# Kernel tuning notes

Measured on AMD Instinct MI355X. Metric: run time of the kernel, lower is better.

Reference implementation:

```python
import jax, jax.numpy as jnp
import numpy as np

N, E, B = 50000, 800000, 64
IN, H, OUT = 64, 128, 64


def _gcn_norm(edge_index, num_nodes):
    # PyG gcn_norm with add_self_loops=True: A_hat = A + I, norm = d^-1/2[src]*d^-1/2[dst]
    loop = jnp.arange(num_nodes)
    src = jnp.concatenate([edge_index[0], loop])
    dst = jnp.concatenate([edge_index[1], loop])
    deg = jax.ops.segment_sum(jnp.ones_like(dst, dtype=jnp.float32), dst,
                              num_segments=num_nodes)  # >= 1 due to self-loops
    dis = deg ** -0.5
    norm = dis[src] * dis[dst]  # [E+N]
    return src, dst, norm


def _gcn_layer(x, W, b, src, dst, norm, num_nodes):
    h = x @ W                                   # linear first (GCNConv order)
    msg = h[src] * norm[:, None]                # gather + normalize, [E+N, H]
    out = jax.ops.segment_sum(msg, dst, num_segments=num_nodes)  # scatter-add
    return out + b


def setup_inputs() -> dict:
    key = jax.random.key(0)
    ks = jax.random.split(key, 12)
    x = jax.random.normal(ks[0], (N, IN), dtype=jnp.float32)
    edge_index = jax.random.randint(ks[1], (2, E), 0, N, dtype=jnp.int64)
    batch = jnp.sort(jax.random.randint(ks[2], (N,), 0, B, dtype=jnp.int64))

    def lin(k, fan_in, fan_out):
        s = 1.0 / np.sqrt(fan_in)
        return jax.random.uniform(k, (fan_in, fan_out), jnp.float32, -s, s)

    return {
        "x": x, "edge_index": edge_index, "batch": batch,
        "W1": lin(ks[3], IN, H), "b1": jnp.zeros((H,), jnp.float32),
        "W2": lin(ks[4], H, H),  "b2": jnp.zeros((H,), jnp.float32),
        "W3": lin(ks[5], H, H),  "b3": jnp.zeros((H,), jnp.float32),
        "W4": lin(ks[6], H, OUT), "b4": jnp.zeros((OUT,), jnp.float32),
    }


def reference(x, edge_index, batch, W1, b1, W2, b2, W3, b3, W4, b4):
    src, dst, norm = _gcn_norm(edge_index, N)
    h = jax.nn.relu(_gcn_layer(x, W1, b1, src, dst, norm, N))
    h = jax.nn.relu(_gcn_layer(h, W2, b2, src, dst, norm, N))
    # global mean pool over graphs
    sums = jax.ops.segment_sum(h, batch, num_segments=B)          # [B, H]
    cnts = jax.ops.segment_sum(jnp.ones((N,), jnp.float32), batch, num_segments=B)
    pooled = sums / jnp.maximum(cnts, 1.0)[:, None]
    # MLP head
    return jax.nn.relu(pooled @ W3 + b3) @ W4 + b4                # [B, OUT]
```

## Files before the change

kernel.cpp:

```cpp
#include <hip/hip_runtime.h>


__device__ __forceinline__ float ldf(const void* p, long long i, int f32) {
    if (f32) return ((const float*)p)[i];
    unsigned int u = ((const unsigned short*)p)[i];
    return __uint_as_float(u << 16);
}
__device__ __forceinline__ float bfl(unsigned int u) { return __uint_as_float(u << 16); }
__device__ __forceinline__ float bfh(unsigned int u) { return __uint_as_float(u & 0xFFFF0000u); }
__device__ __forceinline__ int ld_idx(const int* p, long long i, int i64) {
    return i64 ? p[2 * i] : p[i];
}
__device__ __forceinline__ unsigned short f2bf(float v) {
    unsigned int x = __float_as_uint(v);
    return (unsigned short)((x + 0x7FFFu + ((x >> 16) & 1u)) >> 16);
}
__device__ __forceinline__ int clampi(int v, int lo, int hi) {
    return v < lo ? lo : (v > hi ? hi : v);
}

#define OW1 0
#define OB1 8192
#define OW2 8320
#define OB2 24704
#define OW3 24832
#define OB3 41216
#define OW4 41344
#define OB4 49536
#define OTOT 49600


__global__ void gnn_prep(const void* W1, const void* b1, const void* W2, const void* b2,
                         const void* W3, const void* b3, const void* W4, const void* b4,
                         const int* __restrict__ ei,
                         int* __restrict__ flags_out,
                         int* __restrict__ degcnt, float* __restrict__ pooled,
                         float* __restrict__ wsW, int N, int B) {
    __shared__ int s_cnt, s_or;
    const int t = threadIdx.x;
    if (t == 0) { s_cnt = 0; s_or = 0; }
    __syncthreads();
    {
        const unsigned int* w1w = (const unsigned int*)W1;
        int c = 0, o = 0;
        for (int i = t; i < 512; i += 256) {
            unsigned int e = (w1w[i] >> 7) & 0xFFu;
            if (e >= 100 && e <= 140) c++;
        }
        for (int i = t; i < 1024; i += 256) o |= ei[2 * i + 1];
        atomicAdd(&s_cnt, c);
        atomicOr(&s_or, o);
    }
    __syncthreads();
    const int f32 = (s_cnt > 256) ? 0 : 1;
    if (blockIdx.x == 0 && t == 0) {
        flags_out[0] = f32;
        flags_out[1] = (s_or == 0) ? 1 : 0;
    }
    const int i = blockIdx.x * 256 + t;
    const int stride = gridDim.x * 256;
    for (int j = i; j < N; j += stride) degcnt[j] = 0;
    for (int j = i; j < B * 128; j += stride) pooled[j] = 0.f;
    for (int j = i; j < OTOT; j += stride) {
        float v;
        if      (j < OB1) v = ldf(W1, j - OW1, f32);
        else if (j < OW2) v = ldf(b1, j - OB1, f32);
        else if (j < OB2) v = ldf(W2, j - OW2, f32);
        else if (j < OW3) v = ldf(b2, j - OB2, f32);
        else if (j < OB3) v = ldf(W3, j - OW3, f32);
        else if (j < OW4) v = ldf(b3, j - OB3, f32);
        else if (j < OB4) v = ldf(W4, j - OW4, f32);
        else              v = ldf(b4, j - OB4, f32);
        wsW[j] = v;
    }
}


__global__ void gnn_hist(const int* __restrict__ ei, int E, int N,
                         const int* __restrict__ flags, int* __restrict__ degcnt,
                         int* __restrict__ rank) {
    int base = (blockIdx.x * 256 + threadIdx.x) * 4;
    if (base >= E) return;
    int i64 = flags[1];
    int m = min(4, E - base);
    int d[4], r[4];
#pragma unroll
    for (int j = 0; j < 4; ++j)
        if (j < m) d[j] = clampi(ld_idx(ei, (long long)E + base + j, i64), 0, N - 1);
#pragma unroll
    for (int j = 0; j < 4; ++j)
        if (j < m) r[j] = atomicAdd(&degcnt[d[j]], 1);
#pragma unroll
    for (int j = 0; j < 4; ++j)
        if (j < m) rank[base + j] = r[j];
}

__global__ void gnn_scan1(const int* __restrict__ cnt, int* __restrict__ excl,
                          int* __restrict__ sums, float* __restrict__ dis, int N) {
    __shared__ int sh[256];
    int t = threadIdx.x;
    int i = blockIdx.x * 256 + t;
    int v = (i < N) ? cnt[i] : 0;
    sh[t] = v;
    __syncthreads();
    for (int off = 1; off < 256; off <<= 1) {
        int a = (t >= off) ? sh[t - off] : 0;
        __syncthreads();
        sh[t] += a;
        __syncthreads();
    }
    if (i < N) {
        excl[i] = sh[t] - v;
        dis[i] = rsqrtf((float)v + 1.0f);
    }
    if (t == 255) sums[blockIdx.x] = sh[255];
}

__global__ void gnn_scan2(int* __restrict__ sums, int nb) {
    __shared__ int sh[256];
    int t = threadIdx.x;
    int v = (t < nb) ? sums[t] : 0;
    sh[t] = v;
    __syncthreads();
    for (int off = 1; off < 256; off <<= 1) {
        int a = (t >= off) ? sh[t - off] : 0;
        __syncthreads();
        sh[t] += a;
        __syncthreads();
    }
    if (t < nb) sums[t] = sh[t] - v;
}

template <bool SMALLN>
__global__ void gnn_fill(const int* __restrict__ ei, const int* __restrict__ excl,
                         const int* __restrict__ bsums, const int* __restrict__ rank,
                         void* __restrict__ csr, int E, int N,
                         const int* __restrict__ flags,
                         const void* __restrict__ x, const float* __restrict__ dis,
                         unsigned short* __restrict__ xb) {
    const int tid = blockIdx.x * 256 + threadIdx.x;
    const int i64 = flags[1];
    if (tid < E) {
        int s = clampi(ld_idx(ei, (long long)tid, i64), 0, N - 1);
        int d = clampi(ld_idx(ei, (long long)E + tid, i64), 0, N - 1);
        int pos = excl[d] + bsums[d >> 8] + rank[tid];
        if (SMALLN) ((unsigned short*)csr)[pos] = (unsigned short)s;
        else        ((int*)csr)[pos] = s;
    }
    const int f32 = flags[0];
    const int total = N * 16;
    const int stride = gridDim.x * 256;
    for (int j = tid; j < total; j += stride) {
        int n = j >> 4;
        float dn = dis[n];
        float v0, v1, v2, v3;
        if (f32) {
            float4 xv = ((const float4*)x)[j];
            v0 = xv.x; v1 = xv.y; v2 = xv.z; v3 = xv.w;
        } else {
            ushort4 xv = ((const ushort4*)x)[j];
            v0 = bfl(xv.x); v1 = bfl(xv.y); v2 = bfl(xv.z); v3 = bfl(xv.w);
        }
        ushort4 o;
        o.x = f2bf(v0 * dn); o.y = f2bf(v1 * dn);
        o.z = f2bf(v2 * dn); o.w = f2bf(v3 * dn);
        ((ushort4*)xb)[j] = o;
    }
}

template <bool SMALLN>
__device__ __forceinline__ int csr_at(const void* csr, int e) {
    return SMALLN ? (int)((const unsigned short*)csr)[e] : ((const int*)csr)[e];
}


template <bool SMALLN>
__global__ __launch_bounds__(128) void gnn_l1(const unsigned short* __restrict__ xb,
                                              const int* __restrict__ excl,
                                              const int* __restrict__ bsums,
                                              const void* __restrict__ csr,
                                              const float* __restrict__ dis,
                                              const float* __restrict__ W1,
                                              const float* __restrict__ b1,
                                              int N, int E,
                                              unsigned short* __restrict__ H1b) {
    __shared__ float Xs[16 * 64];
    const int t = threadIdx.x;
    const int nbase = blockIdx.x * 16;
    const int wave = t >> 6;
    const int lane = t & 63;
    const int eslot = lane >> 3;
    const int fg = lane & 7;

    for (int pass = 0; pass < 8; ++pass) {
        const int ln = pass * 2 + wave;
        const int n = nbase + ln;
        float a0 = 0.f, a1 = 0.f, a2 = 0.f, a3 = 0.f;
        float a4 = 0.f, a5 = 0.f, a6 = 0.f, a7 = 0.f;
        if (n < N) {
            int beg = excl[n] + bsums[n >> 8];
            int end = (n + 1 < N) ? (excl[n + 1] + bsums[(n + 1) >> 8]) : E;
            for (int e = beg + eslot; e < end; e += 8) {
                int s = csr_at<SMALLN>(csr, e);
                uint4 u = *(const uint4*)(xb + (long long)s * 64 + fg * 8);
                a0 += bfl(u.x); a1 += bfh(u.x);
                a2 += bfl(u.y); a3 += bfh(u.y);
                a4 += bfl(u.z); a5 += bfh(u.z);
                a6 += bfl(u.w); a7 += bfh(u.w);
            }
        }
#pragma unroll
        for (int m = 8; m <= 32; m <<= 1) {
            a0 += __shfl_xor(a0, m); a1 += __shfl_xor(a1, m);
            a2 += __shfl_xor(a2, m); a3 += __shfl_xor(a3, m);
            a4 += __shfl_xor(a4, m); a5 += __shfl_xor(a5, m);
            a6 += __shfl_xor(a6, m); a7 += __shfl_xor(a7, m);
        }
        if (n < N && eslot == 0) {
            float dn = dis[n];
            uint4 u = *(const uint4*)(xb + (long long)n * 64 + fg * 8);
            float4 o0, o1;
            o0.x = (a0 + bfl(u.x)) * dn; o0.y = (a1 + bfh(u.x)) * dn;
            o0.z = (a2 + bfl(u.y)) * dn; o0.w = (a3 + bfh(u.y)) * dn;
            o1.x = (a4 + bfl(u.z)) * dn; o1.y = (a5 + bfh(u.z)) * dn;
            o1.z = (a6 + bfl(u.w)) * dn; o1.w = (a7 + bfh(u.w)) * dn;
            *(float4*)&Xs[ln * 64 + fg * 8]     = o0;
            *(float4*)&Xs[ln * 64 + fg * 8 + 4] = o1;
        } else if (n >= N && eslot == 0) {
            float4 z = make_float4(0.f, 0.f, 0.f, 0.f);
            *(float4*)&Xs[ln * 64 + fg * 8]     = z;
            *(float4*)&Xs[ln * 64 + fg * 8 + 4] = z;
        }
    }
    __syncthreads();

    const int fgB = t & 31, ng = t >> 5;
    const int f0 = fgB * 4, n0 = ng * 4;
    const float4* Xs4 = (const float4*)Xs;
    const float4* Wp  = (const float4*)W1;
    float4 acc[4];
#pragma unroll
    for (int j = 0; j < 4; ++j) acc[j] = make_float4(0.f, 0.f, 0.f, 0.f);
#pragma unroll 4
    for (int k4 = 0; k4 < 16; ++k4) {
        const float4 wa = Wp[(4 * k4 + 0) * 32 + fgB];
        const float4 wb = Wp[(4 * k4 + 1) * 32 + fgB];
        const float4 wc = Wp[(4 * k4 + 2) * 32 + fgB];
        const float4 wd = Wp[(4 * k4 + 3) * 32 + fgB];
#pragma unroll
        for (int j = 0; j < 4; ++j) {
            const float4 xv = Xs4[(n0 + j) * 16 + k4];
            acc[j].x = fmaf(xv.x, wa.x, acc[j].x); acc[j].y = fmaf(xv.x, wa.y, acc[j].y);
            acc[j].z = fmaf(xv.x, wa.z, acc[j].z); acc[j].w = fmaf(xv.x, wa.w, acc[j].w);
            acc[j].x = fmaf(xv.y, wb.x, acc[j].x); acc[j].y = fmaf(xv.y, wb.y, acc[j].y);
            acc[j].z = fmaf(xv.y, wb.z, acc[j].z); acc[j].w = fmaf(xv.y, wb.w, acc[j].w);
            acc[j].x = fmaf(xv.z, wc.x, acc[j].x); acc[j].y = fmaf(xv.z, wc.y, acc[j].y);
            acc[j].z = fmaf(xv.z, wc.z, acc[j].z); acc[j].w = fmaf(xv.z, wc.w, acc[j].w);
            acc[j].x = fmaf(xv.w, wd.x, acc[j].x); acc[j].y = fmaf(xv.w, wd.y, acc[j].y);
            acc[j].z = fmaf(xv.w, wd.z, acc[j].z); acc[j].w = fmaf(xv.w, wd.w, acc[j].w);
        }
    }
    const float4 b = *(const float4*)&b1[f0];
#pragma unroll
    for (int j = 0; j < 4; ++j) {
        int n = nbase + n0 + j;
        if (n >= N) continue;
        const float dn = dis[n];
        float4 a = acc[j];
        a.x = fmaxf(a.x + b.x, 0.f) * dn;
        a.y = fmaxf(a.y + b.y, 0.f) * dn;
        a.z = fmaxf(a.z + b.z, 0.f) * dn;
        a.w = fmaxf(a.w + b.w, 0.f) * dn;
        uint2 u;
        u.x = (unsigned int)f2bf(a.x) | ((unsigned int)f2bf(a.y) << 16);
        u.y = (unsigned int)f2bf(a.z) | ((unsigned int)f2bf(a.w) << 16);
        *(uint2*)(H1b + (long long)n * 128 + f0) = u;
    }
}


template <bool SMALLN>
__global__ __launch_bounds__(256) void gnn_agg_bf(const unsigned short* __restrict__ H1b,
                                                  const int* __restrict__ excl,
                                                  const int* __restrict__ bsums,
                                                  const void* __restrict__ csr,
                                                  const float* __restrict__ dis,
                                                  float* __restrict__ G, int N, int E) {
    const int t = threadIdx.x;
    const int lane = t & 63;
    const int n = blockIdx.x * 4 + (t >> 6);
    if (n >= N) return;
    const int eslot = lane >> 4;
    const int fg = lane & 15;
    float a0 = 0.f, a1 = 0.f, a2 = 0.f, a3 = 0.f;
    float a4 = 0.f, a5 = 0.f, a6 = 0.f, a7 = 0.f;
    if (eslot == 3) {
        uint4 us = *(const uint4*)(H1b + (long long)n * 128 + fg * 8);
        a0 = bfl(us.x); a1 = bfh(us.x); a2 = bfl(us.y); a3 = bfh(us.y);
        a4 = bfl(us.z); a5 = bfh(us.z); a6 = bfl(us.w); a7 = bfh(us.w);
    }
    int beg = excl[n] + bsums[n >> 8];
    int end = (n + 1 < N) ? (excl[n + 1] + bsums[(n + 1) >> 8]) : E;
    for (int e = beg + eslot; e < end; e += 4) {
        int s = csr_at<SMALLN>(csr, e);
        uint4 u = *(const uint4*)(H1b + (long long)s * 128 + fg * 8);
        a0 += bfl(u.x); a1 += bfh(u.x);
        a2 += bfl(u.y); a3 += bfh(u.y);
        a4 += bfl(u.z); a5 += bfh(u.z);
        a6 += bfl(u.w); a7 += bfh(u.w);
    }
#pragma unroll
    for (int m = 16; m <= 32; m <<= 1) {
        a0 += __shfl_xor(a0, m); a1 += __shfl_xor(a1, m);
        a2 += __shfl_xor(a2, m); a3 += __shfl_xor(a3, m);
        a4 += __shfl_xor(a4, m); a5 += __shfl_xor(a5, m);
        a6 += __shfl_xor(a6, m); a7 += __shfl_xor(a7, m);
    }
    if (eslot == 0) {
        const float dn = dis[n];
        float4 o0, o1;
        o0.x = a0 * dn; o0.y = a1 * dn; o0.z = a2 * dn; o0.w = a3 * dn;
        o1.x = a4 * dn; o1.y = a5 * dn; o1.z = a6 * dn; o1.w = a7 * dn;
        *(float4*)(G + (long long)n * 128 + fg * 8)     = o0;
        *(float4*)(G + (long long)n * 128 + fg * 8 + 4) = o1;
    }
}


__global__ __launch_bounds__(128) void gnn_lin2pool(const float* __restrict__ X,
                                                    const float* __restrict__ Wf,
                                                    const float* __restrict__ bias,
                                                    const int* __restrict__ batch,
                                                    const int* __restrict__ flags,
                                                    float* __restrict__ pooled,
                                                    int N, int B) {
    __shared__ float Xs[16 * 128];
    __shared__ float Rs[4 * 128];
    __shared__ int s_uni;
    const int t = threadIdx.x;
    const int nbase = blockIdx.x * 16;
    const int i64 = flags[1];

    if (t == 0) {
        int nlast = min(nbase + 15, N - 1);
        int bfirst = clampi(ld_idx(batch, nbase, i64), 0, B - 1);
        int blast  = clampi(ld_idx(batch, nlast, i64), 0, B - 1);
        s_uni = (bfirst == blast) ? (bfirst + 1) : 0;
    }

#pragma unroll
    for (int it = 0; it < 4; ++it) {
        int i4 = t + it * 128;
        int n = nbase + (i4 * 4) / 128;
        float4 v = make_float4(0.f, 0.f, 0.f, 0.f);
        if (n < N) v = ((const float4*)X)[(long long)nbase * 32 + i4];
        ((float4*)Xs)[i4] = v;
    }
    __syncthreads();

    const int fg = t & 31, ng = t >> 5;
    const int f0 = fg * 4, n0 = ng * 4;
    const float4* Xs4 = (const float4*)Xs;
    const float4* Wp  = (const float4*)Wf;
    float4 acc[4];
#pragma unroll
    for (int j = 0; j < 4; ++j) acc[j] = make_float4(0.f, 0.f, 0.f, 0.f);
#pragma unroll 4
    for (int k4 = 0; k4 < 32; ++k4) {
        const float4 wa = Wp[(4 * k4 + 0) * 32 + fg];
        const float4 wb = Wp[(4 * k4 + 1) * 32 + fg];
        const float4 wc = Wp[(4 * k4 + 2) * 32 + fg];
        const float4 wd = Wp[(4 * k4 + 3) * 32 + fg];
#pragma unroll
        for (int j = 0; j < 4; ++j) {
            const float4 xv = Xs4[(n0 + j) * 32 + k4];
            acc[j].x = fmaf(xv.x, wa.x, acc[j].x); acc[j].y = fmaf(xv.x, wa.y, acc[j].y);
            acc[j].z = fmaf(xv.x, wa.z, acc[j].z); acc[j].w = fmaf(xv.x, wa.w, acc[j].w);
            acc[j].x = fmaf(xv.y, wb.x, acc[j].x); acc[j].y = fmaf(xv.y, wb.y, acc[j].y);
            acc[j].z = fmaf(xv.y, wb.z, acc[j].z); acc[j].w = fmaf(xv.y, wb.w, acc[j].w);
            acc[j].x = fmaf(xv.z, wc.x, acc[j].x); acc[j].y = fmaf(xv.z, wc.y, acc[j].y);
            acc[j].z = fmaf(xv.z, wc.z, acc[j].z); acc[j].w = fmaf(xv.z, wc.w, acc[j].w);
            acc[j].x = fmaf(xv.w, wd.x, acc[j].x); acc[j].y = fmaf(xv.w, wd.y, acc[j].y);
            acc[j].z = fmaf(xv.w, wd.z, acc[j].z); acc[j].w = fmaf(xv.w, wd.w, acc[j].w);
        }
    }
    const float4 b = *(const float4*)&bias[f0];
    if (s_uni) {
        const int bb = s_uni - 1;
        float4 s = make_float4(0.f, 0.f, 0.f, 0.f);
#pragma unroll
        for (int j = 0; j < 4; ++j) {
            int n = nbase + n0 + j;
            if (n >= N) break;
            float4 a = acc[j];
            s.x += fmaxf(a.x + b.x, 0.f);
            s.y += fmaxf(a.y + b.y, 0.f);
            s.z += fmaxf(a.z + b.z, 0.f);
            s.w += fmaxf(a.w + b.w, 0.f);
        }
        *(float4*)&Rs[ng * 128 + f0] = s;
        __syncthreads();
        if (ng == 0) {
            float4 s0 = *(const float4*)&Rs[0 * 128 + f0];
            float4 s1 = *(const float4*)&Rs[1 * 128 + f0];
            float4 s2 = *(const float4*)&Rs[2 * 128 + f0];
            float4 s3 = *(const float4*)&Rs[3 * 128 + f0];
            float4 tt;
            tt.x = s0.x + s1.x + s2.x + s3.x;
            tt.y = s0.y + s1.y + s2.y + s3.y;
            tt.z = s0.z + s1.z + s2.z + s3.z;
            tt.w = s0.w + s1.w + s2.w + s3.w;
            float* pp = &pooled[bb * 128 + f0];
            atomicAdd(pp + 0, tt.x); atomicAdd(pp + 1, tt.y);
            atomicAdd(pp + 2, tt.z); atomicAdd(pp + 3, tt.w);
        }
    } else {
        int bprev = -1;
        float4 s = make_float4(0.f, 0.f, 0.f, 0.f);
#pragma unroll
        for (int j = 0; j < 4; ++j) {
            int n = nbase + n0 + j;
            if (n >= N) break;
            float4 a = acc[j];
            a.x = fmaxf(a.x + b.x, 0.f);
            a.y = fmaxf(a.y + b.y, 0.f);
            a.z = fmaxf(a.z + b.z, 0.f);
            a.w = fmaxf(a.w + b.w, 0.f);
            int bj = clampi(ld_idx(batch, n, i64), 0, B - 1);
            if (bj != bprev) {
                if (bprev >= 0) {
                    float* pp = &pooled[bprev * 128 + f0];
                    atomicAdd(pp + 0, s.x); atomicAdd(pp + 1, s.y);
                    atomicAdd(pp + 2, s.z); atomicAdd(pp + 3, s.w);
                }
                s = a; bprev = bj;
            } else {
                s.x += a.x; s.y += a.y; s.z += a.z; s.w += a.w;
            }
        }
        if (bprev >= 0) {
            float* pp = &pooled[bprev * 128 + f0];
            atomicAdd(pp + 0, s.x); atomicAdd(pp + 1, s.y);
            atomicAdd(pp + 2, s.z); atomicAdd(pp + 3, s.w);
        }
    }
}


__global__ __launch_bounds__(128) void gnn_head(const float* __restrict__ pooled,
                                                const int* __restrict__ batch,
                                                const float* __restrict__ W3,
                                                const float* __restrict__ b3,
                                                const float* __restrict__ W4,
                                                const float* __restrict__ b4,
                                                const int* __restrict__ flags,
                                                void* __restrict__ outv, int N) {
    __shared__ float xs[128];
    __shared__ float rs[128];
    __shared__ float cinv;
    int b = blockIdx.x, f = threadIdx.x;
    if (f == 0) {
        int i64 = flags[1];
        int L = 0, R = N;
        while (L < R) { int m = (L + R) >> 1; if (ld_idx(batch, m, i64) < b) L = m + 1; else R = m; }
        int lo = L;
        L = 0; R = N;
        while (L < R) { int m = (L + R) >> 1; if (ld_idx(batch, m, i64) < b + 1) L = m + 1; else R = m; }
        cinv = 1.0f / fmaxf((float)(L - lo), 1.0f);
    }
    __syncthreads();
    xs[f] = pooled[b * 128 + f] * cinv;
    __syncthreads();
    float acc = b3[f];
    for (int k = 0; k < 128; ++k) acc = fmaf(xs[k], W3[k * 128 + f], acc);
    rs[f] = fmaxf(acc, 0.f);
    __syncthreads();
    if (f < 64) {
        float a2 = b4[f];
        for (int k = 0; k < 128; ++k) a2 = fmaf(rs[k], W4[k * 64 + f], a2);
        if (flags[0]) ((float*)outv)[b * 64 + f] = a2;
        else          ((unsigned short*)outv)[b * 64 + f] = f2bf(a2);
    }
}


extern "C" void kernel_launch(void* const* d_in, const int* in_sizes, int n_in,
                              void* d_out, int out_size, void* d_ws, size_t ws_size,
                              hipStream_t stream) {
    const void* x  = d_in[0];
    const int* ei  = (const int*)d_in[1];
    const int* bat = (const int*)d_in[2];

    const int N = in_sizes[0] / 64;
    const int E = in_sizes[1] / 2;
    const int B = out_size / 64;
    const bool smalln = (N < 65536);

    char* p = (char*)d_ws;
    auto alloc = [&](size_t bytes) { void* q = (void*)p; p += (bytes + 255) & ~(size_t)255; return q; };
    int*   flags    = (int*)alloc(256);
    float* wsW      = (float*)alloc((size_t)OTOT * 4);
    int*   degcnt   = (int*)alloc((size_t)N * 4);
    float* dis      = (float*)alloc((size_t)N * 4);
    int*   excl     = (int*)alloc((size_t)N * 4);
    int*   bsums    = (int*)alloc(1024);
    int*   rank     = (int*)alloc((size_t)E * 4);
    void*  csr      = alloc((size_t)E * (smalln ? 2 : 4));
    unsigned short* xb  = (unsigned short*)alloc((size_t)N * 64 * 2);
    unsigned short* H1b = (unsigned short*)alloc((size_t)N * 128 * 2);
    float* G        = (float*)alloc((size_t)N * 128 * 4);
    float* pooled   = (float*)alloc((size_t)B * 128 * 4);
    (void)ws_size; (void)n_in;

    const int nbN = (N + 255) / 256;

    gnn_prep<<<512, 256, 0, stream>>>(d_in[3], d_in[4], d_in[5], d_in[6],
                                      d_in[7], d_in[8], d_in[9], d_in[10],
                                      ei, flags, degcnt, pooled, wsW, N, B);

    gnn_hist<<<(E + 1023) / 1024, 256, 0, stream>>>(ei, E, N, flags, degcnt, rank);
    gnn_scan1<<<nbN, 256, 0, stream>>>(degcnt, excl, bsums, dis, N);
    gnn_scan2<<<1, 256, 0, stream>>>(bsums, nbN);
    if (smalln)
        gnn_fill<true><<<(E + 255) / 256, 256, 0, stream>>>(ei, excl, bsums, rank, csr, E, N,
                                                            flags, x, dis, xb);
    else
        gnn_fill<false><<<(E + 255) / 256, 256, 0, stream>>>(ei, excl, bsums, rank, csr, E, N,
                                                             flags, x, dis, xb);

    const int nblk = (N + 15) / 16;

    if (smalln)
        gnn_l1<true><<<nblk, 128, 0, stream>>>(xb, excl, bsums, csr, dis,
                                               wsW + OW1, wsW + OB1, N, E, H1b);
    else
        gnn_l1<false><<<nblk, 128, 0, stream>>>(xb, excl, bsums, csr, dis,
                                                wsW + OW1, wsW + OB1, N, E, H1b);

    if (smalln)
        gnn_agg_bf<true><<<(N + 3) / 4, 256, 0, stream>>>(H1b, excl, bsums, csr, dis, G, N, E);
    else
        gnn_agg_bf<false><<<(N + 3) / 4, 256, 0, stream>>>(H1b, excl, bsums, csr, dis, G, N, E);

    gnn_lin2pool<<<nblk, 128, 0, stream>>>(G, wsW + OW2, wsW + OB2, bat, flags, pooled, N, B);

    gnn_head<<<B, 128, 0, stream>>>(pooled, bat, wsW + OW3, wsW + OB3,
                                    wsW + OW4, wsW + OB4, flags, d_out, N);
}
```

Baseline: 272.9 us.

## Fuse layer-2 aggregation with linear transform and mean pooling

Merges the layer-2 neighbour aggregation kernel into the linear+pool kernel. Each 256-thread block now aggregates its 16 nodes into shared memory, then multiplies by W2 staged in shared-memory chunks and pools. This removes the fp32 G intermediate (N×128 floats written and read back) and one kernel launch. In exchange, each wave runs four sequential aggregation passes, the block needs more shared memory, and the GEMM loop adds extra barriers, which may reduce occupancy and latency hiding.

```diff
diff --git a/kernel.cpp b/kernel.cpp
--- a/kernel.cpp
+++ b/kernel.cpp
@@ -280,62 +280,20 @@
 
 
 template <bool SMALLN>
-__global__ __launch_bounds__(256) void gnn_agg_bf(const unsigned short* __restrict__ H1b,
-                                                  const int* __restrict__ excl,
-                                                  const int* __restrict__ bsums,
-                                                  const void* __restrict__ csr,
-                                                  const float* __restrict__ dis,
-                                                  float* __restrict__ G, int N, int E) {
-    const int t = threadIdx.x;
-    const int lane = t & 63;
-    const int n = blockIdx.x * 4 + (t >> 6);
-    if (n >= N) return;
-    const int eslot = lane >> 4;
-    const int fg = lane & 15;
-    float a0 = 0.f, a1 = 0.f, a2 = 0.f, a3 = 0.f;
-    float a4 = 0.f, a5 = 0.f, a6 = 0.f, a7 = 0.f;
-    if (eslot == 3) {
-        uint4 us = *(const uint4*)(H1b + (long long)n * 128 + fg * 8);
-        a0 = bfl(us.x); a1 = bfh(us.x); a2 = bfl(us.y); a3 = bfh(us.y);
-        a4 = bfl(us.z); a5 = bfh(us.z); a6 = bfl(us.w); a7 = bfh(us.w);
-    }
-    int beg = excl[n] + bsums[n >> 8];
-    int end = (n + 1 < N) ? (excl[n + 1] + bsums[(n + 1) >> 8]) : E;
-    for (int e = beg + eslot; e < end; e += 4) {
-        int s = csr_at<SMALLN>(csr, e);
-        uint4 u = *(const uint4*)(H1b + (long long)s * 128 + fg * 8);
-        a0 += bfl(u.x); a1 += bfh(u.x);
-        a2 += bfl(u.y); a3 += bfh(u.y);
-        a4 += bfl(u.z); a5 += bfh(u.z);
-        a6 += bfl(u.w); a7 += bfh(u.w);
-    }
-#pragma unroll
-    for (int m = 16; m <= 32; m <<= 1) {
-        a0 += __shfl_xor(a0, m); a1 += __shfl_xor(a1, m);
-        a2 += __shfl_xor(a2, m); a3 += __shfl_xor(a3, m);
-        a4 += __shfl_xor(a4, m); a5 += __shfl_xor(a5, m);
-        a6 += __shfl_xor(a6, m); a7 += __shfl_xor(a7, m);
-    }
-    if (eslot == 0) {
-        const float dn = dis[n];
-        float4 o0, o1;
-        o0.x = a0 * dn; o0.y = a1 * dn; o0.z = a2 * dn; o0.w = a3 * dn;
-        o1.x = a4 * dn; o1.y = a5 * dn; o1.z = a6 * dn; o1.w = a7 * dn;
-        *(float4*)(G + (long long)n * 128 + fg * 8)     = o0;
-        *(float4*)(G + (long long)n * 128 + fg * 8 + 4) = o1;
-    }
-}
-
-
-__global__ __launch_bounds__(128) void gnn_lin2pool(const float* __restrict__ X,
-                                                    const float* __restrict__ Wf,
-                                                    const float* __restrict__ bias,
-                                                    const int* __restrict__ batch,
-                                                    const int* __restrict__ flags,
-                                                    float* __restrict__ pooled,
-                                                    int N, int B) {
+__global__ __launch_bounds__(256) void gnn_l2(const unsigned short* __restrict__ H1b,
+                                              const int* __restrict__ excl,
+                                              const int* __restrict__ bsums,
+                                              const void* __restrict__ csr,
+                                              const float* __restrict__ dis,
+                                              const float* __restrict__ W2,
+                                              const float* __restrict__ b2,
+                                              const int* __restrict__ batch,
+                                              const int* __restrict__ flags,
+                                              float* __restrict__ pooled,
+                                              int N, int E, int B) {
     __shared__ float Xs[16 * 128];
-    __shared__ float Rs[4 * 128];
+    __shared__ float Wc[32 * 128];
+    __shared__ float Rs[8 * 128];
     __shared__ int s_uni;
     const int t = threadIdx.x;
     const int nbase = blockIdx.x * 16;
@@ -348,48 +306,90 @@
         s_uni = (bfirst == blast) ? (bfirst + 1) : 0;
     }
 
-#pragma unroll
-    for (int it = 0; it < 4; ++it) {
-        int i4 = t + it * 128;
-        int n = nbase + (i4 * 4) / 128;
-        float4 v = make_float4(0.f, 0.f, 0.f, 0.f);
-        if (n < N) v = ((const float4*)X)[(long long)nbase * 32 + i4];
-        ((float4*)Xs)[i4] = v;
+    {
+        const int wave = t >> 6;
+        const int lane = t & 63;
+        const int eslot = lane >> 4;
+        const int fgA = lane & 15;
+        for (int pass = 0; pass < 4; ++pass) {
+            const int nd = pass * 4 + wave;
+            const int n = nbase + nd;
+            float a0 = 0.f, a1 = 0.f, a2 = 0.f, a3 = 0.f;
+            float a4 = 0.f, a5 = 0.f, a6 = 0.f, a7 = 0.f;
+            if (n < N) {
+                if (eslot == 3) {
+                    uint4 us = *(const uint4*)(H1b + (long long)n * 128 + fgA * 8);
+                    a0 = bfl(us.x); a1 = bfh(us.x); a2 = bfl(us.y); a3 = bfh(us.y);
+                    a4 = bfl(us.z); a5 = bfh(us.z); a6 = bfl(us.w); a7 = bfh(us.w);
+                }
+                int beg = excl[n] + bsums[n >> 8];
+                int end = (n + 1 < N) ? (excl[n + 1] + bsums[(n + 1) >> 8]) : E;
+                for (int e = beg + eslot; e < end; e += 4) {
+                    int s = csr_at<SMALLN>(csr, e);
+                    uint4 u = *(const uint4*)(H1b + (long long)s * 128 + fgA * 8);
+                    a0 += bfl(u.x); a1 += bfh(u.x);
+                    a2 += bfl(u.y); a3 += bfh(u.y);
+                    a4 += bfl(u.z); a5 += bfh(u.z);
+                    a6 += bfl(u.w); a7 += bfh(u.w);
+                }
+            }
+#pragma unroll
+            for (int m = 16; m <= 32; m <<= 1) {
+                a0 += __shfl_xor(a0, m); a1 += __shfl_xor(a1, m);
+                a2 += __shfl_xor(a2, m); a3 += __shfl_xor(a3, m);
+                a4 += __shfl_xor(a4, m); a5 += __shfl_xor(a5, m);
+                a6 += __shfl_xor(a6, m); a7 += __shfl_xor(a7, m);
+            }
+            if (eslot == 0) {
+                const float dn = (n < N) ? dis[n] : 0.f;
+                float4 o0, o1;
+                o0.x = a0 * dn; o0.y = a1 * dn; o0.z = a2 * dn; o0.w = a3 * dn;
+                o1.x = a4 * dn; o1.y = a5 * dn; o1.z = a6 * dn; o1.w = a7 * dn;
+                *(float4*)&Xs[nd * 128 + fgA * 8]     = o0;
+                *(float4*)&Xs[nd * 128 + fgA * 8 + 4] = o1;
+            }
+        }
     }
     __syncthreads();
 
     const int fg = t & 31, ng = t >> 5;
-    const int f0 = fg * 4, n0 = ng * 4;
-    const float4* Xs4 = (const float4*)Xs;
-    const float4* Wp  = (const float4*)Wf;
-    float4 acc[4];
-#pragma unroll
-    for (int j = 0; j < 4; ++j) acc[j] = make_float4(0.f, 0.f, 0.f, 0.f);
-#pragma unroll 4
-    for (int k4 = 0; k4 < 32; ++k4) {
-        const float4 wa = Wp[(4 * k4 + 0) * 32 + fg];
-        const float4 wb = Wp[(4 * k4 + 1) * 32 + fg];
-        const float4 wc = Wp[(4 * k4 + 2) * 32 + fg];
-        const float4 wd = Wp[(4 * k4 + 3) * 32 + fg];
-#pragma unroll
-        for (int j = 0; j < 4; ++j) {
-            const float4 xv = Xs4[(n0 + j) * 32 + k4];
-            acc[j].x = fmaf(xv.x, wa.x, acc[j].x); acc[j].y = fmaf(xv.x, wa.y, acc[j].y);
-            acc[j].z = fmaf(xv.x, wa.z, acc[j].z); acc[j].w = fmaf(xv.x, wa.w, acc[j].w);
-            acc[j].x = fmaf(xv.y, wb.x, acc[j].x); acc[j].y = fmaf(xv.y, wb.y, acc[j].y);
-            acc[j].z = fmaf(xv.y, wb.z, acc[j].z); acc[j].w = fmaf(xv.y, wb.w, acc[j].w);
-            acc[j].x = fmaf(xv.z, wc.x, acc[j].x); acc[j].y = fmaf(xv.z, wc.y, acc[j].y);
-            acc[j].z = fmaf(xv.z, wc.z, acc[j].z); acc[j].w = fmaf(xv.z, wc.w, acc[j].w);
-            acc[j].x = fmaf(xv.w, wd.x, acc[j].x); acc[j].y = fmaf(xv.w, wd.y, acc[j].y);
-            acc[j].z = fmaf(xv.w, wd.z, acc[j].z); acc[j].w = fmaf(xv.w, wd.w, acc[j].w);
-        }
-    }
-    const float4 b = *(const float4*)&bias[f0];
+    const int f0 = fg * 4, n0 = ng * 2;
+    float4 acc[2];
+    acc[0] = make_float4(0.f, 0.f, 0.f, 0.f);
+    acc[1] = make_float4(0.f, 0.f, 0.f, 0.f);
+    for (int c = 0; c < 4; ++c) {
+#pragma unroll
+        for (int i = 0; i < 4; ++i)
+            ((float4*)Wc)[t + i * 256] = ((const float4*)(W2 + c * 32 * 128))[t + i * 256];
+        __syncthreads();
+#pragma unroll
+        for (int k4r = 0; k4r < 8; ++k4r) {
+            const float4 wa = ((const float4*)Wc)[(4 * k4r + 0) * 32 + fg];
+            const float4 wb = ((const float4*)Wc)[(4 * k4r + 1) * 32 + fg];
+            const float4 wc2 = ((const float4*)Wc)[(4 * k4r + 2) * 32 + fg];
+            const float4 wd = ((const float4*)Wc)[(4 * k4r + 3) * 32 + fg];
+#pragma unroll
+            for (int j = 0; j < 2; ++j) {
+                const float4 xv = ((const float4*)Xs)[(n0 + j) * 32 + c * 8 + k4r];
+                acc[j].x = fmaf(xv.x, wa.x, acc[j].x); acc[j].y = fmaf(xv.x, wa.y, acc[j].y);
+                acc[j].z = fmaf(xv.x, wa.z, acc[j].z); acc[j].w = fmaf(xv.x, wa.w, acc[j].w);
+                acc[j].x = fmaf(xv.y, wb.x, acc[j].x); acc[j].y = fmaf(xv.y, wb.y, acc[j].y);
+                acc[j].z = fmaf(xv.y, wb.z, acc[j].z); acc[j].w = fmaf(xv.y, wb.w, acc[j].w);
+                acc[j].x = fmaf(xv.z, wc2.x, acc[j].x); acc[j].y = fmaf(xv.z, wc2.y, acc[j].y);
+                acc[j].z = fmaf(xv.z, wc2.z, acc[j].z); acc[j].w = fmaf(xv.z, wc2.w, acc[j].w);
+                acc[j].x = fmaf(xv.w, wd.x, acc[j].x); acc[j].y = fmaf(xv.w, wd.y, acc[j].y);
+                acc[j].z = fmaf(xv.w, wd.z, acc[j].z); acc[j].w = fmaf(xv.w, wd.w, acc[j].w);
+            }
+        }
+        __syncthreads();
+    }
+
+    const float4 b = *(const float4*)&b2[f0];
     if (s_uni) {
         const int bb = s_uni - 1;
         float4 s = make_float4(0.f, 0.f, 0.f, 0.f);
 #pragma unroll
-        for (int j = 0; j < 4; ++j) {
+        for (int j = 0; j < 2; ++j) {
             int n = nbase + n0 + j;
             if (n >= N) break;
             float4 a = acc[j];
@@ -401,15 +401,12 @@
         *(float4*)&Rs[ng * 128 + f0] = s;
         __syncthreads();
         if (ng == 0) {
-            float4 s0 = *(const float4*)&Rs[0 * 128 + f0];
-            float4 s1 = *(const float4*)&Rs[1 * 128 + f0];
-            float4 s2 = *(const float4*)&Rs[2 * 128 + f0];
-            float4 s3 = *(const float4*)&Rs[3 * 128 + f0];
-            float4 tt;
-            tt.x = s0.x + s1.x + s2.x + s3.x;
-            tt.y = s0.y + s1.y + s2.y + s3.y;
-            tt.z = s0.z + s1.z + s2.z + s3.z;
-            tt.w = s0.w + s1.w + s2.w + s3.w;
+            float4 tt = make_float4(0.f, 0.f, 0.f, 0.f);
+#pragma unroll
+            for (int g = 0; g < 8; ++g) {
+                float4 sg = *(const float4*)&Rs[g * 128 + f0];
+                tt.x += sg.x; tt.y += sg.y; tt.z += sg.z; tt.w += sg.w;
+            }
             float* pp = &pooled[bb * 128 + f0];
             atomicAdd(pp + 0, tt.x); atomicAdd(pp + 1, tt.y);
             atomicAdd(pp + 2, tt.z); atomicAdd(pp + 3, tt.w);
@@ -418,7 +415,7 @@
         int bprev = -1;
         float4 s = make_float4(0.f, 0.f, 0.f, 0.f);
 #pragma unroll
-        for (int j = 0; j < 4; ++j) {
+        for (int j = 0; j < 2; ++j) {
             int n = nbase + n0 + j;
             if (n >= N) break;
             float4 a = acc[j];
@@ -508,7 +505,6 @@
     void*  csr      = alloc((size_t)E * (smalln ? 2 : 4));
     unsigned short* xb  = (unsigned short*)alloc((size_t)N * 64 * 2);
     unsigned short* H1b = (unsigned short*)alloc((size_t)N * 128 * 2);
-    float* G        = (float*)alloc((size_t)N * 128 * 4);
     float* pooled   = (float*)alloc((size_t)B * 128 * 4);
     (void)ws_size; (void)n_in;
 
@@ -538,11 +534,13 @@
                                                 wsW + OW1, wsW + OB1, N, E, H1b);
 
     if (smalln)
-        gnn_agg_bf<true><<<(N + 3) / 4, 256, 0, stream>>>(H1b, excl, bsums, csr, dis, G, N, E);
+        gnn_l2<true><<<nblk, 256, 0, stream>>>(H1b, excl, bsums, csr, dis,
+                                               wsW + OW2, wsW + OB2, bat, flags,
+                                               pooled, N, E, B);
     else
-        gnn_agg_bf<false><<<(N + 3) / 4, 256, 0, stream>>>(H1b, excl, bsums, csr, dis, G, N, E);
-
-    gnn_lin2pool<<<nblk, 128, 0, stream>>>(G, wsW + OW2, wsW + OB2, bat, flags, pooled, N, B);
+        gnn_l2<false><<<nblk, 256, 0, stream>>>(H1b, excl, bsums, csr, dis,
+                                                wsW + OW2, wsW + OB2, bat, flags,
+                                                pooled, N, E, B);
 
     gnn_head<<<B, 128, 0, stream>>>(pooled, bat, wsW + OW3, wsW + OB3,
                                     wsW + OW4, wsW + OB4, flags, d_out, N);
```

Result: slower. 291.2 us (+6.7%).
